# Performance work log

Hardware: AMD Instinct MI355X
Metric: run time of the kernel (lower is better)

Reference implementation:

```python
import jax, jax.numpy as jnp
import numpy as np

HIDDEN = 1024
NUM_HEADS = 16
D_HEAD = HIDDEN // NUM_HEADS  # 64
SEQ = 2048
BATCH = 2


def setup_inputs() -> dict:
    key = jax.random.key(0)
    kx, kw, kb = jax.random.split(key, 3)
    x = jax.random.normal(kx, (SEQ, BATCH, HIDDEN), dtype=jnp.float32)
    W = jax.random.normal(kw, (3 * HIDDEN, HIDDEN), dtype=jnp.float32) * 0.02
    b = jax.random.normal(kb, (3 * HIDDEN,), dtype=jnp.float32) * 0.02
    return {"x": x, "W": W, "b": b}


def reference(x, W, b):
    # x: (S, B, H) seq-first, as in the torch module
    S, B, _ = x.shape
    qkv = jnp.einsum('sbh,oh->sbo', x, W) + b  # (S, B, 3*H)
    # torch views 3*hidden as (num_heads, 3, d_head): per-head-interleaved QKV
    qkv = qkv.reshape(S, B, NUM_HEADS, 3, D_HEAD)
    qkv = jnp.transpose(qkv, (2, 1, 0, 3, 4))  # (nh, B, S, 3, d)
    q, k, v = qkv[..., 0, :], qkv[..., 1, :], qkv[..., 2, :]  # each (nh, B, S, d)
    scale = 1.0 / np.sqrt(D_HEAD).astype(np.float32)
    scores = jnp.einsum('hbqd,hbkd->hbqk', q, k) * scale  # (nh, B, S, S)
    attn = jax.nn.softmax(scores, axis=-1)
    out = jnp.einsum('hbqk,hbkd->hbqd', attn, v)  # (nh, B, S, d)
    out = jnp.transpose(out, (2, 1, 0, 3)).reshape(S, B, HIDDEN)
    return out
```

## Files before the change

kernel.cpp:

```cpp
#include <hip/hip_runtime.h>
#include <hip/hip_bf16.h>


typedef __hip_bfloat16 bf16;
typedef __bf16 bfr;
typedef __attribute__((ext_vector_type(8))) __bf16 bf16x8;
typedef __attribute__((ext_vector_type(4))) __bf16 bf16x4;
typedef __attribute__((ext_vector_type(2))) __bf16 bf16x2;
typedef __attribute__((ext_vector_type(4))) float f32x4;
typedef __attribute__((ext_vector_type(16))) float f32x16;
typedef __attribute__((ext_vector_type(4))) unsigned u32x4;

#define S_SEQ  2048
#define HID    1024
#define OUT3   3072
#define NROWS  4096

#if __has_builtin(__builtin_amdgcn_exp2f)
#define EXP2F(x) __builtin_amdgcn_exp2f(x)
#else
#define EXP2F(x) exp2f(x)
#endif

#define QSCALE 0.18033688011112042f

__global__ __launch_bounds__(256) void cast_both_kernel(
    const float* __restrict__ X, bfr* __restrict__ Xb,
    const float* __restrict__ W, bfr* __restrict__ Wb)
{
    int bid = blockIdx.x;
    const float* src;
    bfr* dst;
    int lid;
    if (bid < NROWS * HID / 2048) { src = X; dst = Xb; lid = bid; }
    else { src = W; dst = Wb; lid = bid - NROWS * HID / 2048; }
    int gid = lid * 256 + threadIdx.x;
    const float4* s4 = (const float4*)src;
    float4 a = s4[(size_t)gid * 2];
    float4 b = s4[(size_t)gid * 2 + 1];
    bf16x8 v;
    v[0] = (bfr)a.x; v[1] = (bfr)a.y; v[2] = (bfr)a.z; v[3] = (bfr)a.w;
    v[4] = (bfr)b.x; v[5] = (bfr)b.y; v[6] = (bfr)b.z; v[7] = (bfr)b.w;
    *(bf16x8*)(dst + (size_t)gid * 8) = v;
}

__device__ __forceinline__ void gload_lds16(const void* g, void* l) {
    __builtin_amdgcn_global_load_lds(
        (const __attribute__((address_space(1))) unsigned int*)g,
        (__attribute__((address_space(3))) unsigned int*)l, 16, 0, 0);
}

__global__ __launch_bounds__(256, 3) void qkv_gemm_mfma(
    const bfr* __restrict__ Xb, const bfr* __restrict__ Wb,
    const float* __restrict__ bias,
    bfr* __restrict__ qb, bfr* __restrict__ kb, bfr* __restrict__ vtb)
{
    __shared__ __attribute__((aligned(16))) unsigned char lds_all[32768];
    bfr* As = (bfr*)lds_all;
    bfr* Bs = (bfr*)(lds_all + 16384);
    bfr* Tr = (bfr*)lds_all;

    const int o0 = blockIdx.x * 128;
    const int r0 = blockIdx.y * 128;
    const int tid = threadIdx.x;
    const int lane = tid & 63;
    const int w = tid >> 6;
    const int l15 = lane & 15;
    const int quad = lane >> 4;
    const int m0 = (w & 1) * 64;
    const int n0 = (w >> 1) * 64;

    f32x4 acc[4][4];
#pragma unroll
    for (int mi = 0; mi < 4; mi++)
#pragma unroll
        for (int ni = 0; ni < 4; ni++) acc[mi][ni] = {0.f, 0.f, 0.f, 0.f};

    for (int k0 = 0; k0 < HID; k0 += 64) {
#pragma unroll
        for (int i = 0; i < 4; i++) {
            int c = i * 256 + tid;
            int row = c >> 3, c8 = c & 7;
            gload_lds16(Xb + (size_t)(r0 + row) * HID + k0 + c8 * 8, As + c * 8);
            gload_lds16(Wb + (size_t)(o0 + row) * HID + k0 + c8 * 8, Bs + c * 8);
        }
        __syncthreads();

#pragma unroll
        for (int ks = 0; ks < 2; ks++) {
            bf16x8 af[4], bfg[4];
#pragma unroll
            for (int mi = 0; mi < 4; mi++)
                af[mi] = *(const bf16x8*)(As + (m0 + mi * 16 + l15) * 64 + ks * 32 + quad * 8);
#pragma unroll
            for (int ni = 0; ni < 4; ni++)
                bfg[ni] = *(const bf16x8*)(Bs + (n0 + ni * 16 + l15) * 64 + ks * 32 + quad * 8);
#pragma unroll
            for (int mi = 0; mi < 4; mi++)
#pragma unroll
                for (int ni = 0; ni < 4; ni++)
                    acc[mi][ni] = __builtin_amdgcn_mfma_f32_16x16x32_bf16(
                        af[mi], bfg[ni], acc[mi][ni], 0, 0, 0);
        }
        __syncthreads();
    }

    const int omod = o0 % 192;
#pragma unroll
    for (int ni = 0; ni < 4; ni++) {
        int cb = o0 + n0 + ni * 16;
        int h = cb / 192;
        int rem = cb % 192;
        int t = rem >> 6;
        int d = (rem & 63) + l15;
        float bv = bias[cb + l15];
        if (t == 2) {
#pragma unroll
            for (int mi = 0; mi < 4; mi++)
#pragma unroll
                for (int r = 0; r < 4; r++) {
                    int grl = m0 + mi * 16 + quad * 4 + r;
                    Tr[(size_t)d * 144 + (grl & 1) * 72 + (grl >> 1)]
                        = (bfr)(acc[mi][ni][r] + bv);
                }
        } else {
#pragma unroll
            for (int mi = 0; mi < 4; mi++)
#pragma unroll
                for (int r = 0; r < 4; r++) {
                    int gr = r0 + m0 + mi * 16 + quad * 4 + r;
                    int s = gr >> 1, b = gr & 1;
                    int hb = h * 2 + b;
                    float val = acc[mi][ni][r] + bv;
                    if (t == 0)
                        qb[((size_t)hb * S_SEQ + s) * 64 + d] = (bfr)(val * QSCALE);
                    else
                        kb[((size_t)hb * S_SEQ + s) * 64 + d] = (bfr)val;
                }
        }
    }
    if (omod != 0) {
        __syncthreads();
        int ht = (omod == 64) ? (o0 + 64) / 192 : o0 / 192;
        int d = tid >> 2;
        int b = (tid >> 1) & 1;
        int chunk = tid & 1;
        int s0 = r0 >> 1;
        int hb = ht * 2 + b;
        const bfr* src = Tr + (size_t)d * 144 + b * 72 + chunk * 32;
        bfr* dstp = vtb + ((size_t)hb * 64 + d) * S_SEQ + s0 + chunk * 32;
#pragma unroll
        for (int j = 0; j < 4; j++)
            *(bf16x8*)(dstp + j * 8) = *(const bf16x8*)(src + j * 8);
    }
}

__device__ __forceinline__ void plswap(unsigned &a, unsigned &b) {
    asm volatile("v_permlane32_swap_b32 %0, %1" : "+v"(a), "+v"(b));
}

__global__ __launch_bounds__(256, 2) void attn32_kernel(
    const bfr* __restrict__ qb, const bfr* __restrict__ kb,
    const bfr* __restrict__ vtb, float* __restrict__ out)
{
    __shared__ __attribute__((aligned(16))) bfr KV[4][2][64 * 64];

    const int qt = blockIdx.x;
    const int hb = blockIdx.y;
    const int h = hb >> 1, b = hb & 1;
    const int tid = threadIdx.x;
    const int lane = tid & 63;
    const int w = tid >> 6;
    const int l31 = lane & 31;
    const int hi = lane >> 5;
    const size_t hboff = (size_t)hb * S_SEQ * 64;

    const int srow = tid >> 3;
    const int slot = tid & 7;

    const int qrow = qt * 128 + w * 32 + l31;
    bf16x8 qf[4];
#pragma unroll
    for (int kk = 0; kk < 4; kk++)
        qf[kk] = *(const bf16x8*)(qb + hboff + (size_t)qrow * 64 + kk * 16 + hi * 8);

    f32x16 Oacc[2];
#pragma unroll
    for (int dt = 0; dt < 2; dt++)
#pragma unroll
        for (int i = 0; i < 16; i++) Oacc[dt][i] = 0.f;
    float lsum = 0.f;

#define STAGE(kt_, buf_) do {                                                  \
    int kt__ = (kt_); int bf__ = (buf_);                                       \
    _Pragma("unroll")                                                          \
    for (int i = 0; i < 2; i++) {                                              \
        int r = i * 32 + srow;                                                 \
        int gc = slot ^ (r & 7);                                               \
        gload_lds16(kb + hboff + (size_t)(kt__ * 64 + r) * 64 + gc * 8,        \
                    (bfr*)&KV[bf__][0][0] + i * 2048 + tid * 8);               \
    }                                                                          \
    _Pragma("unroll")                                                          \
    for (int i = 0; i < 2; i++) {                                              \
        int r = i * 32 + srow;                                                 \
        int gc = slot ^ (r & 7);                                               \
        gload_lds16(vtb + hboff + (size_t)r * S_SEQ + kt__ * 64 + gc * 8,      \
                    (bfr*)&KV[bf__][1][0] + i * 2048 + tid * 8);               \
    }                                                                          \
} while (0)

    STAGE(0, 0);
    STAGE(1, 1);

    for (int kt = 0; kt < 32; kt++) {
        {
            int ktn = (kt + 2 <= 31) ? kt + 2 : 31;
            STAGE(ktn, (kt + 2) & 3);
        }
        asm volatile("s_waitcnt vmcnt(8)" ::: "memory");
        __builtin_amdgcn_s_barrier();

        const bfr* Kb = &KV[kt & 3][0][0];
        const bfr* Vb = &KV[kt & 3][1][0];

        unsigned wds[2][8];
        float rs = 0.f;
#pragma unroll
        for (int t = 0; t < 2; t++) {
            f32x16 sc;
#pragma unroll
            for (int i = 0; i < 16; i++) sc[i] = 0.f;
#pragma unroll
            for (int kk = 0; kk < 4; kk++) {
                int krow = t * 32 + l31;
                int ks = (kk * 2 + hi) ^ (krow & 7);
                bf16x8 kf = *(const bf16x8*)(Kb + krow * 64 + ks * 8);
                sc = __builtin_amdgcn_mfma_f32_32x32x16_bf16(kf, qf[kk], sc, 0, 0, 0);
            }
#pragma unroll
            for (int a = 0; a < 8; a++) {
                float p0 = EXP2F(sc[2 * a]);
                float p1 = EXP2F(sc[2 * a + 1]);
                rs += p0 + p1;
                bf16x2 pk; pk[0] = (bfr)p0; pk[1] = (bfr)p1;
                wds[t][a] = __builtin_bit_cast(unsigned, pk);
            }
        }
        lsum += rs;

        bf16x8 pfrag[4];
#pragma unroll
        for (int c = 0; c < 4; c++) {
            int t = c >> 1, cc = c & 1;
            unsigned w0 = wds[t][cc * 4 + 0];
            unsigned w1 = wds[t][cc * 4 + 1];
            unsigned w2 = wds[t][cc * 4 + 2];
            unsigned w3 = wds[t][cc * 4 + 3];
            plswap(w0, w2);
            plswap(w1, w3);
            u32x4 pw; pw[0] = w0; pw[1] = w1; pw[2] = w2; pw[3] = w3;
            pfrag[c] = __builtin_bit_cast(bf16x8, pw);
        }

#pragma unroll
        for (int kk = 0; kk < 4; kk++)
#pragma unroll
            for (int dt = 0; dt < 2; dt++) {
                int vrow = dt * 32 + l31;
                int vs = (kk * 2 + hi) ^ (vrow & 7);
                bf16x8 vf = *(const bf16x8*)(Vb + vrow * 64 + vs * 8);
                Oacc[dt] = __builtin_amdgcn_mfma_f32_32x32x16_bf16(vf, pfrag[kk], Oacc[dt], 0, 0, 0);
            }
    }
#undef STAGE

    lsum += __shfl_xor(lsum, 32);
    float inv = 1.0f / lsum;
    float* orow = out + ((size_t)qrow * 2 + b) * HID + h * 64;
#pragma unroll
    for (int dt = 0; dt < 2; dt++)
#pragma unroll
        for (int g = 0; g < 4; g++) {
            float4 o4;
            o4.x = Oacc[dt][4 * g + 0] * inv;
            o4.y = Oacc[dt][4 * g + 1] * inv;
            o4.z = Oacc[dt][4 * g + 2] * inv;
            o4.w = Oacc[dt][4 * g + 3] * inv;
            *(float4*)(orow + dt * 32 + 8 * g + 4 * hi) = o4;
        }
}

extern "C" void kernel_launch(void* const* d_in, const int* in_sizes, int n_in,
                              void* d_out, int out_size, void* d_ws, size_t ws_size,
                              hipStream_t stream) {
    const float* X    = (const float*)d_in[0];
    const float* W    = (const float*)d_in[1];
    const float* bias = (const float*)d_in[2];
    float* out = (float*)d_out;

    bfr* qb  = (bfr*)d_ws;
    bfr* kb  = qb + (size_t)32 * S_SEQ * 64;
    bfr* vtb = kb + (size_t)32 * S_SEQ * 64;

    bfr* Xb = (bfr*)d_out;
    bfr* Wb = Xb + (size_t)NROWS * HID;

    cast_both_kernel<<<(NROWS * HID + OUT3 * HID) / 2048, 256, 0, stream>>>(X, Xb, W, Wb);

    dim3 g1(OUT3 / 128, NROWS / 128);
    qkv_gemm_mfma<<<g1, 256, 0, stream>>>(Xb, Wb, bias, qb, kb, vtb);

    dim3 g2(S_SEQ / 128, 32);
    attn32_kernel<<<g2, 256, 0, stream>>>(qb, kb, vtb, out);
}
```

Baseline: 157.7 us.

## Process two KV tiles per barrier and raise MFMA priority with setprio

Restructures the attention inner loop so each iteration handles two 64-key tiles, with one vmcnt(0) wait and one barrier per pair instead of per tile. Prefetch of the next two tiles is issued right after the barrier into the 4-slot ring. s_setprio brackets the MFMA sections so they are favoured over other waves. The aim is fewer barriers and more MFMA work per synchronization point. In exchange it needs more registers for the larger wds and pfrag arrays, and it has a full vmcnt(0) drain where the old loop left loads outstanding.

```diff
diff --git a/kernel.cpp b/kernel.cpp
--- a/kernel.cpp
+++ b/kernel.cpp
@@ -191,8 +191,8 @@
         for (int i = 0; i < 16; i++) Oacc[dt][i] = 0.f;
     float lsum = 0.f;
 
-#define STAGE(kt_, buf_) do {                                                  \
-    int kt__ = (kt_); int bf__ = (buf_);                                       \
+#define STAGE(kt_) do {                                                        \
+    int kt__ = (kt_); int bf__ = kt__ & 3;                                     \
     _Pragma("unroll")                                                          \
     for (int i = 0; i < 2; i++) {                                              \
         int r = i * 32 + srow;                                                 \
@@ -209,34 +209,32 @@
     }                                                                          \
 } while (0)
 
-    STAGE(0, 0);
-    STAGE(1, 1);
-
-    for (int kt = 0; kt < 32; kt++) {
-        {
-            int ktn = (kt + 2 <= 31) ? kt + 2 : 31;
-            STAGE(ktn, (kt + 2) & 3);
-        }
-        asm volatile("s_waitcnt vmcnt(8)" ::: "memory");
+    STAGE(0);
+    STAGE(1);
+
+    for (int it = 0; it < 16; it++) {
+        const int t0 = 2 * it;
+        asm volatile("s_waitcnt vmcnt(0)" ::: "memory");
         __builtin_amdgcn_s_barrier();
-
-        const bfr* Kb = &KV[kt & 3][0][0];
-        const bfr* Vb = &KV[kt & 3][1][0];
-
-        unsigned wds[2][8];
+        if (it < 15) { STAGE(t0 + 2); STAGE(t0 + 3); }
+
+        unsigned wds[4][8];
         float rs = 0.f;
 #pragma unroll
-        for (int t = 0; t < 2; t++) {
+        for (int t = 0; t < 4; t++) {
+            const bfr* Kb = &KV[(t0 + (t >> 1)) & 3][0][0];
+            const int krow = (t & 1) * 32 + l31;
             f32x16 sc;
 #pragma unroll
             for (int i = 0; i < 16; i++) sc[i] = 0.f;
+            __builtin_amdgcn_s_setprio(1);
 #pragma unroll
             for (int kk = 0; kk < 4; kk++) {
-                int krow = t * 32 + l31;
                 int ks = (kk * 2 + hi) ^ (krow & 7);
                 bf16x8 kf = *(const bf16x8*)(Kb + krow * 64 + ks * 8);
                 sc = __builtin_amdgcn_mfma_f32_32x32x16_bf16(kf, qf[kk], sc, 0, 0, 0);
             }
+            __builtin_amdgcn_s_setprio(0);
 #pragma unroll
             for (int a = 0; a < 8; a++) {
                 float p0 = EXP2F(sc[2 * a]);
@@ -248,9 +246,9 @@
         }
         lsum += rs;
 
-        bf16x8 pfrag[4];
-#pragma unroll
-        for (int c = 0; c < 4; c++) {
+        bf16x8 pfrag[8];
+#pragma unroll
+        for (int c = 0; c < 8; c++) {
             int t = c >> 1, cc = c & 1;
             unsigned w0 = wds[t][cc * 4 + 0];
             unsigned w1 = wds[t][cc * 4 + 1];
@@ -262,15 +260,20 @@
             pfrag[c] = __builtin_bit_cast(bf16x8, pw);
         }
 
-#pragma unroll
-        for (int kk = 0; kk < 4; kk++)
+        __builtin_amdgcn_s_setprio(1);
+#pragma unroll
+        for (int kk = 0; kk < 8; kk++) {
+            const bfr* Vb = &KV[(t0 + (kk >> 2)) & 3][1][0];
+            const int kkl = kk & 3;
 #pragma unroll
             for (int dt = 0; dt < 2; dt++) {
                 int vrow = dt * 32 + l31;
-                int vs = (kk * 2 + hi) ^ (vrow & 7);
+                int vs = (kkl * 2 + hi) ^ (vrow & 7);
                 bf16x8 vf = *(const bf16x8*)(Vb + vrow * 64 + vs * 8);
                 Oacc[dt] = __builtin_amdgcn_mfma_f32_32x32x16_bf16(vf, pfrag[kk], Oacc[dt], 0, 0, 0);
             }
+        }
+        __builtin_amdgcn_s_setprio(0);
     }
 #undef STAGE
 
```

After: 154.9 us. Within noise of the previous version (-1.8%).

## Split attention KV range across two blocks with atomic-flag combine

Applied to the files above, without the earlier changes.

Splits each query tile's 32 key tiles across two blocks (split-K), doubling the attention grid. Each block writes unnormalized partial outputs and row sums to workspace, and the second block to finish (found through an atomic counter that the cast kernel zeroes) merges the partials and normalizes. It also cuts LDS buffering from four stages to two and raises the occupancy hint to 4 blocks per CU to improve latency hiding. The cost is extra global traffic for partials and less prefetch depth, and the split path only runs if the workspace is large enough.

```diff
diff --git a/kernel.cpp b/kernel.cpp
--- a/kernel.cpp
+++ b/kernel.cpp
@@ -26,9 +26,14 @@
 
 __global__ __launch_bounds__(256) void cast_both_kernel(
     const float* __restrict__ X, bfr* __restrict__ Xb,
-    const float* __restrict__ W, bfr* __restrict__ Wb)
+    const float* __restrict__ W, bfr* __restrict__ Wb,
+    int* flags)
 {
     int bid = blockIdx.x;
+    if (flags != nullptr && bid == 0) {
+        flags[threadIdx.x] = 0;
+        flags[threadIdx.x + 256] = 0;
+    }
     const float* src;
     bfr* dst;
     int lid;
@@ -159,13 +164,19 @@
     asm volatile("v_permlane32_swap_b32 %0, %1" : "+v"(a), "+v"(b));
 }
 
-__global__ __launch_bounds__(256, 2) void attn32_kernel(
+template<int NSPLIT>
+__global__ __launch_bounds__(256, 4) void attn32_kernel(
     const bfr* __restrict__ qb, const bfr* __restrict__ kb,
-    const bfr* __restrict__ vtb, float* __restrict__ out)
+    const bfr* __restrict__ vtb,
+    float* po, float* lsumP, int* flags,
+    float* __restrict__ out)
 {
-    __shared__ __attribute__((aligned(16))) bfr KV[4][2][64 * 64];
-
-    const int qt = blockIdx.x;
+    __shared__ __attribute__((aligned(16))) bfr KV[2][2][64 * 64];
+
+    constexpr int NT = 32 / NSPLIT;
+    const int qt    = (NSPLIT == 2) ? (blockIdx.x >> 1) : blockIdx.x;
+    const int split = (NSPLIT == 2) ? (blockIdx.x & 1) : 0;
+    const int tbase = split * NT;
     const int hb = blockIdx.y;
     const int h = hb >> 1, b = hb & 1;
     const int tid = threadIdx.x;
@@ -191,8 +202,8 @@
         for (int i = 0; i < 16; i++) Oacc[dt][i] = 0.f;
     float lsum = 0.f;
 
-#define STAGE(kt_, buf_) do {                                                  \
-    int kt__ = (kt_); int bf__ = (buf_);                                       \
+#define STAGE(lt_) do {                                                        \
+    int lt__ = (lt_); int kt__ = tbase + lt__; int bf__ = lt__ & 1;            \
     _Pragma("unroll")                                                          \
     for (int i = 0; i < 2; i++) {                                              \
         int r = i * 32 + srow;                                                 \
@@ -209,30 +220,26 @@
     }                                                                          \
 } while (0)
 
-    STAGE(0, 0);
-    STAGE(1, 1);
-
-    for (int kt = 0; kt < 32; kt++) {
-        {
-            int ktn = (kt + 2 <= 31) ? kt + 2 : 31;
-            STAGE(ktn, (kt + 2) & 3);
-        }
-        asm volatile("s_waitcnt vmcnt(8)" ::: "memory");
+    STAGE(0);
+
+    for (int t = 0; t < NT; t++) {
+        asm volatile("s_waitcnt vmcnt(0)" ::: "memory");
         __builtin_amdgcn_s_barrier();
-
-        const bfr* Kb = &KV[kt & 3][0][0];
-        const bfr* Vb = &KV[kt & 3][1][0];
+        if (t + 1 < NT) STAGE(t + 1);
+
+        const bfr* Kb = &KV[t & 1][0][0];
+        const bfr* Vb = &KV[t & 1][1][0];
 
         unsigned wds[2][8];
         float rs = 0.f;
 #pragma unroll
-        for (int t = 0; t < 2; t++) {
+        for (int ts = 0; ts < 2; ts++) {
+            const int krow = ts * 32 + l31;
             f32x16 sc;
 #pragma unroll
             for (int i = 0; i < 16; i++) sc[i] = 0.f;
 #pragma unroll
             for (int kk = 0; kk < 4; kk++) {
-                int krow = t * 32 + l31;
                 int ks = (kk * 2 + hi) ^ (krow & 7);
                 bf16x8 kf = *(const bf16x8*)(Kb + krow * 64 + ks * 8);
                 sc = __builtin_amdgcn_mfma_f32_32x32x16_bf16(kf, qf[kk], sc, 0, 0, 0);
@@ -243,7 +250,7 @@
                 float p1 = EXP2F(sc[2 * a + 1]);
                 rs += p0 + p1;
                 bf16x2 pk; pk[0] = (bfr)p0; pk[1] = (bfr)p1;
-                wds[t][a] = __builtin_bit_cast(unsigned, pk);
+                wds[ts][a] = __builtin_bit_cast(unsigned, pk);
             }
         }
         lsum += rs;
@@ -251,11 +258,11 @@
         bf16x8 pfrag[4];
 #pragma unroll
         for (int c = 0; c < 4; c++) {
-            int t = c >> 1, cc = c & 1;
-            unsigned w0 = wds[t][cc * 4 + 0];
-            unsigned w1 = wds[t][cc * 4 + 1];
-            unsigned w2 = wds[t][cc * 4 + 2];
-            unsigned w3 = wds[t][cc * 4 + 3];
+            int ts = c >> 1, cc = c & 1;
+            unsigned w0 = wds[ts][cc * 4 + 0];
+            unsigned w1 = wds[ts][cc * 4 + 1];
+            unsigned w2 = wds[ts][cc * 4 + 2];
+            unsigned w3 = wds[ts][cc * 4 + 3];
             plswap(w0, w2);
             plswap(w1, w3);
             u32x4 pw; pw[0] = w0; pw[1] = w1; pw[2] = w2; pw[3] = w3;
@@ -275,19 +282,63 @@
 #undef STAGE
 
     lsum += __shfl_xor(lsum, 32);
-    float inv = 1.0f / lsum;
-    float* orow = out + ((size_t)qrow * 2 + b) * HID + h * 64;
-#pragma unroll
-    for (int dt = 0; dt < 2; dt++)
-#pragma unroll
-        for (int g = 0; g < 4; g++) {
-            float4 o4;
-            o4.x = Oacc[dt][4 * g + 0] * inv;
-            o4.y = Oacc[dt][4 * g + 1] * inv;
-            o4.z = Oacc[dt][4 * g + 2] * inv;
-            o4.w = Oacc[dt][4 * g + 3] * inv;
-            *(float4*)(orow + dt * 32 + 8 * g + 4 * hi) = o4;
-        }
+
+    if constexpr (NSPLIT == 1) {
+        float inv = 1.0f / lsum;
+        float* orow = out + ((size_t)qrow * 2 + b) * HID + h * 64;
+#pragma unroll
+        for (int dt = 0; dt < 2; dt++)
+#pragma unroll
+            for (int g = 0; g < 4; g++) {
+                float4 o4;
+                o4.x = Oacc[dt][4 * g + 0] * inv;
+                o4.y = Oacc[dt][4 * g + 1] * inv;
+                o4.z = Oacc[dt][4 * g + 2] * inv;
+                o4.w = Oacc[dt][4 * g + 3] * inv;
+                *(float4*)(orow + dt * 32 + 8 * g + 4 * hi) = o4;
+            }
+    } else {
+        float* prow = po + (((size_t)split * 32 + hb) * S_SEQ + qrow) * 64;
+#pragma unroll
+        for (int dt = 0; dt < 2; dt++)
+#pragma unroll
+            for (int g = 0; g < 4; g++) {
+                float4 o4;
+                o4.x = Oacc[dt][4 * g + 0];
+                o4.y = Oacc[dt][4 * g + 1];
+                o4.z = Oacc[dt][4 * g + 2];
+                o4.w = Oacc[dt][4 * g + 3];
+                *(float4*)(prow + dt * 32 + 8 * g + 4 * hi) = o4;
+            }
+        if (hi == 0)
+            lsumP[((size_t)split * 32 + hb) * S_SEQ + qrow] = lsum;
+        __threadfence();
+        __syncthreads();
+        __shared__ int role;
+        if (tid == 0) role = atomicAdd(&flags[hb * 16 + qt], 1);
+        __syncthreads();
+        if (role == 1) {
+            __threadfence();
+            const float* qrow2 =
+                po + (((size_t)(1 - split) * 32 + hb) * S_SEQ + qrow) * 64;
+            float l2 = lsumP[((size_t)(1 - split) * 32 + hb) * S_SEQ + qrow];
+            float inv = 1.0f / (lsum + l2);
+            float* orow = out + ((size_t)qrow * 2 + b) * HID + h * 64;
+#pragma unroll
+            for (int dt = 0; dt < 2; dt++)
+#pragma unroll
+                for (int g = 0; g < 4; g++) {
+                    int off = dt * 32 + 8 * g + 4 * hi;
+                    float4 p = *(const float4*)(qrow2 + off);
+                    float4 o4;
+                    o4.x = (Oacc[dt][4 * g + 0] + p.x) * inv;
+                    o4.y = (Oacc[dt][4 * g + 1] + p.y) * inv;
+                    o4.z = (Oacc[dt][4 * g + 2] + p.z) * inv;
+                    o4.w = (Oacc[dt][4 * g + 3] + p.w) * inv;
+                    *(float4*)(orow + off) = o4;
+                }
+        }
+    }
 }
 
 extern "C" void kernel_launch(void* const* d_in, const int* in_sizes, int n_in,
@@ -302,14 +353,30 @@
     bfr* kb  = qb + (size_t)32 * S_SEQ * 64;
     bfr* vtb = kb + (size_t)32 * S_SEQ * 64;
 
+    const size_t qkv_bytes = (size_t)3 * 32 * S_SEQ * 64 * 2;
+    const size_t po_elems  = (size_t)2 * 32 * S_SEQ * 64;
+    const size_t ls_elems  = (size_t)2 * 32 * S_SEQ;
+    const size_t need = qkv_bytes + po_elems * 4 + ls_elems * 4 + 512 * 4;
+    const bool use_split = ws_size >= need;
+
+    float* po    = (float*)((char*)d_ws + qkv_bytes);
+    float* lsumP = po + po_elems;
+    int*   flags = (int*)(lsumP + ls_elems);
+
     bfr* Xb = (bfr*)d_out;
     bfr* Wb = Xb + (size_t)NROWS * HID;
 
-    cast_both_kernel<<<(NROWS * HID + OUT3 * HID) / 2048, 256, 0, stream>>>(X, Xb, W, Wb);
+    cast_both_kernel<<<(NROWS * HID + OUT3 * HID) / 2048, 256, 0, stream>>>(
+        X, Xb, W, Wb, use_split ? flags : nullptr);
 
     dim3 g1(OUT3 / 128, NROWS / 128);
     qkv_gemm_mfma<<<g1, 256, 0, stream>>>(Xb, Wb, bias, qb, kb, vtb);
 
-    dim3 g2(S_SEQ / 128, 32);
-    attn32_kernel<<<g2, 256, 0, stream>>>(qb, kb, vtb, out);
-}
+    if (use_split) {
+        dim3 g2(S_SEQ / 64, 32);
+        attn32_kernel<2><<<g2, 256, 0, stream>>>(qb, kb, vtb, po, lsumP, flags, out);
+    } else {
+        dim3 g2(S_SEQ / 128, 32);
+        attn32_kernel<1><<<g2, 256, 0, stream>>>(qb, kb, vtb, nullptr, nullptr, nullptr, out);
+    }
+}
```

After: 402.6 us. 155% more time.

## Switch attention K/V staging from 4-buffer depth-2 prefetch to double buffering

Applied to the files above, without the earlier changes.

Cuts the LDS K/V ring from four tiles to two and replaces the prefetch-two-ahead scheme (waitcnt vmcnt(8)) with a wait-all, barrier, then issue-next-tile double buffer. This halves shared memory per block, which could allow more resident blocks, and simplifies the buffer indexing. In exchange, each tile's global load now only overlaps one iteration of compute, and the full vmcnt(0) wait can expose load latency.

```diff
diff --git a/kernel.cpp b/kernel.cpp
--- a/kernel.cpp
+++ b/kernel.cpp
@@ -163,8 +163,9 @@
     const bfr* __restrict__ qb, const bfr* __restrict__ kb,
     const bfr* __restrict__ vtb, float* __restrict__ out)
 {
-    __shared__ __attribute__((aligned(16))) bfr KV[4][2][64 * 64];
-
+    __shared__ __attribute__((aligned(16))) bfr KV[2][2][64 * 64];
+
+    constexpr int NT = 32;
     const int qt = blockIdx.x;
     const int hb = blockIdx.y;
     const int h = hb >> 1, b = hb & 1;
@@ -191,8 +192,8 @@
         for (int i = 0; i < 16; i++) Oacc[dt][i] = 0.f;
     float lsum = 0.f;
 
-#define STAGE(kt_, buf_) do {                                                  \
-    int kt__ = (kt_); int bf__ = (buf_);                                       \
+#define STAGE(t_) do {                                                         \
+    int kt__ = (t_); int bf__ = kt__ & 1;                                      \
     _Pragma("unroll")                                                          \
     for (int i = 0; i < 2; i++) {                                              \
         int r = i * 32 + srow;                                                 \
@@ -209,30 +210,26 @@
     }                                                                          \
 } while (0)
 
-    STAGE(0, 0);
-    STAGE(1, 1);
-
-    for (int kt = 0; kt < 32; kt++) {
-        {
-            int ktn = (kt + 2 <= 31) ? kt + 2 : 31;
-            STAGE(ktn, (kt + 2) & 3);
-        }
-        asm volatile("s_waitcnt vmcnt(8)" ::: "memory");
+    STAGE(0);
+
+    for (int t = 0; t < NT; t++) {
+        asm volatile("s_waitcnt vmcnt(0)" ::: "memory");
         __builtin_amdgcn_s_barrier();
-
-        const bfr* Kb = &KV[kt & 3][0][0];
-        const bfr* Vb = &KV[kt & 3][1][0];
+        if (t + 1 < NT) STAGE(t + 1);
+
+        const bfr* Kb = &KV[t & 1][0][0];
+        const bfr* Vb = &KV[t & 1][1][0];
 
         unsigned wds[2][8];
         float rs = 0.f;
 #pragma unroll
-        for (int t = 0; t < 2; t++) {
+        for (int ts = 0; ts < 2; ts++) {
+            const int krow = ts * 32 + l31;
             f32x16 sc;
 #pragma unroll
             for (int i = 0; i < 16; i++) sc[i] = 0.f;
 #pragma unroll
             for (int kk = 0; kk < 4; kk++) {
-                int krow = t * 32 + l31;
                 int ks = (kk * 2 + hi) ^ (krow & 7);
                 bf16x8 kf = *(const bf16x8*)(Kb + krow * 64 + ks * 8);
                 sc = __builtin_amdgcn_mfma_f32_32x32x16_bf16(kf, qf[kk], sc, 0, 0, 0);
@@ -243,7 +240,7 @@
                 float p1 = EXP2F(sc[2 * a + 1]);
                 rs += p0 + p1;
                 bf16x2 pk; pk[0] = (bfr)p0; pk[1] = (bfr)p1;
-                wds[t][a] = __builtin_bit_cast(unsigned, pk);
+                wds[ts][a] = __builtin_bit_cast(unsigned, pk);
             }
         }
         lsum += rs;
@@ -251,11 +248,11 @@
         bf16x8 pfrag[4];
 #pragma unroll
         for (int c = 0; c < 4; c++) {
-            int t = c >> 1, cc = c & 1;
-            unsigned w0 = wds[t][cc * 4 + 0];
-            unsigned w1 = wds[t][cc * 4 + 1];
-            unsigned w2 = wds[t][cc * 4 + 2];
-            unsigned w3 = wds[t][cc * 4 + 3];
+            int ts = c >> 1, cc = c & 1;
+            unsigned w0 = wds[ts][cc * 4 + 0];
+            unsigned w1 = wds[ts][cc * 4 + 1];
+            unsigned w2 = wds[ts][cc * 4 + 2];
+            unsigned w3 = wds[ts][cc * 4 + 3];
             plswap(w0, w2);
             plswap(w1, w3);
             u32x4 pw; pw[0] = w0; pw[1] = w1; pw[2] = w2; pw[3] = w3;
```

Result: no change. 157.7 us (+0.0%).
